# Kernel optimization log

Measured on AMD Instinct MI355X. Metric: run time of the kernel, lower is better.

## Reference

```python
import jax, jax.numpy as jnp
import numpy as np

DECAY = 0.9
THRESH = 1.0
ALPHA = 4.0  # surrogate-gradient sharpness for the LIF heaviside
NUM_HEADS = 8


def lif(x):
    """LIF neuron over leading time axis: mem = decay*mem + x; spike = H(mem - thresh); soft reset.
    Forward emits the hard spike; a sigmoid surrogate carries the gradient (straight-through).
    x: (T, M, D) -> spikes (T, M, D)."""
    def step(mem, xt):
        mem = DECAY * mem + xt
        sg = jax.nn.sigmoid(ALPHA * (mem - THRESH))
        hard = (mem >= THRESH).astype(xt.dtype)
        spike = sg + jax.lax.stop_gradient(hard - sg)
        mem = mem - spike * THRESH
        return mem, spike
    _, spikes = jax.lax.scan(step, jnp.zeros_like(x[0]), x)
    return spikes


def setup_inputs() -> dict:
    key = jax.random.key(0)
    ks = jax.random.split(key, 6)
    T, B, N, D = 4, 16, 1024, 512
    s = 1.0 / np.sqrt(D)
    return {
        "x_seq": jax.random.normal(ks[0], (T, B, N, D), jnp.float32),
        "Wq": (jax.random.normal(ks[1], (D, D), jnp.float32) * s),
        "Wk": (jax.random.normal(ks[2], (D, D), jnp.float32) * s),
        "Wv": (jax.random.normal(ks[3], (D, D), jnp.float32) * s),
        "Wp": (jax.random.normal(ks[4], (D, D), jnp.float32) * s),
        "bp": jnp.zeros((D,), jnp.float32),
    }


def reference(x_seq, Wq, Wk, Wv, Wp, bp):
    T, B, N, D = x_seq.shape
    hd = D // NUM_HEADS
    xf = x_seq.reshape(T, B * N, D)
    # projections (no bias) + LIF spiking, then the module's view into (T,B,H,N,hd)
    q = lif(xf @ Wq.T).reshape(T, B, NUM_HEADS, N, hd)
    k = lif(xf @ Wk.T).reshape(T, B, NUM_HEADS, N, hd)
    v = lif(xf @ Wv.T).reshape(T, B, NUM_HEADS, N, hd)
    # causal linear attention: elementwise kv, cumulative sum over time (kv_state is None on fresh module)
    context = jnp.cumsum(k * v, axis=0)
    out = (q * context).reshape(T, B * N, D)
    return (out @ Wp.T + bp).reshape(T, B, N, D)
```

## Files before the change

kernel.cpp:

```cpp
#include <hip/hip_runtime.h>
#include <hip/hip_bf16.h>
#include <stdint.h>

#define T_ 4
#define M_ 16384
#define D_ 512
#define R_ (T_ * M_)
#define EPS_TRIG 1e-4f

typedef short bf16x8 __attribute__((ext_vector_type(8)));
typedef float f32x4  __attribute__((ext_vector_type(4)));
typedef unsigned short us8 __attribute__((ext_vector_type(8)));

static __device__ __forceinline__ void split2bf16(float x, unsigned short& h, unsigned short& l) {
    unsigned int u = __float_as_uint(x);
    h = (unsigned short)(u >> 16);
    float r = x - __uint_as_float(u & 0xFFFF0000u);
    unsigned int v = __float_as_uint(r);
    l = (unsigned short)((v + 0x7FFFu + ((v >> 16) & 1u)) >> 16);
}

static __device__ __forceinline__ void gload_lds16(const void* g, void* l) {
    __builtin_amdgcn_global_load_lds(
        (const __attribute__((address_space(1))) unsigned int*)g,
        (__attribute__((address_space(3))) unsigned int*)l,
        16, 0, 0);
}

__global__ __launch_bounds__(256) void split_w_tiled(
    const float* __restrict__ Wq, const float* __restrict__ Wk, const float* __restrict__ Wv,
    unsigned short* __restrict__ Wt)
{
    const int flat = blockIdx.x * 256 + threadIdx.x;
    const int dd   = flat & 63;
    const int rest = flat >> 6;
    const int wj   = rest % 24;
    const int bk   = rest / 24;
    const int kbi  = bk & 15;
    const int bd   = bk >> 4;
    const int z    = wj % 3;
    const int hg   = wj / 3;
    const int hl   = hg >> 2;
    const int g    = hg & 3;

    const float* src = ((z == 0) ? Wq : (z == 1) ? Wk : Wv)
                       + (size_t)(bd * 64 + dd) * D_ + kbi * 32 + g * 8;
    float4 a = *reinterpret_cast<const float4*>(src);
    float4 b = *reinterpret_cast<const float4*>(src + 4);

    us8 hv, lv;
    unsigned short hh, ll;
    split2bf16(a.x, hh, ll); hv[0] = hh; lv[0] = ll;
    split2bf16(a.y, hh, ll); hv[1] = hh; lv[1] = ll;
    split2bf16(a.z, hh, ll); hv[2] = hh; lv[2] = ll;
    split2bf16(a.w, hh, ll); hv[3] = hh; lv[3] = ll;
    split2bf16(b.x, hh, ll); hv[4] = hh; lv[4] = ll;
    split2bf16(b.y, hh, ll); hv[5] = hh; lv[5] = ll;
    split2bf16(b.z, hh, ll); hv[6] = hh; lv[6] = ll;
    split2bf16(b.w, hh, ll); hv[7] = hh; lv[7] = ll;

    *reinterpret_cast<us8*>((char*)Wt + (size_t)flat * 16) = hl ? lv : hv;
}

__global__ __launch_bounds__(256) void split_wp_tiled(
    const float* __restrict__ Wp, unsigned short* __restrict__ WpT)
{
    const int flat = blockIdx.x * 256 + threadIdx.x;
    const int dd   = flat & 63;
    const int g    = (flat >> 6) & 3;
    const int kbi  = (flat >> 8) & 15;
    const int bd   = flat >> 12;

    const float* src = Wp + (size_t)(bd * 64 + dd) * D_ + kbi * 32 + g * 8;
    float4 a = *reinterpret_cast<const float4*>(src);
    float4 b = *reinterpret_cast<const float4*>(src + 4);

    us8 hv, lv;
    unsigned short hh, ll;
    split2bf16(a.x, hh, ll); hv[0] = hh; lv[0] = ll;
    split2bf16(a.y, hh, ll); hv[1] = hh; lv[1] = ll;
    split2bf16(a.z, hh, ll); hv[2] = hh; lv[2] = ll;
    split2bf16(a.w, hh, ll); hv[3] = hh; lv[3] = ll;
    split2bf16(b.x, hh, ll); hv[4] = hh; lv[4] = ll;
    split2bf16(b.y, hh, ll); hv[5] = hh; lv[5] = ll;
    split2bf16(b.z, hh, ll); hv[6] = hh; lv[6] = ll;
    split2bf16(b.w, hh, ll); hv[7] = hh; lv[7] = ll;

    char* chunk = (char*)WpT + (size_t)(bd * 16 + kbi) * 8192;
    *reinterpret_cast<us8*>(chunk + g * 1024 + dd * 16)        = hv;
    *reinterpret_cast<us8*>(chunk + 4096 + g * 1024 + dd * 16) = lv;
}

__global__ __launch_bounds__(256) void split_x_tiled3(
    const float* __restrict__ X, unsigned short* __restrict__ Xt)
{
    const int bmp  = blockIdx.x;
    const int tid  = threadIdx.x;
    const int rowp = tid >> 2;
    const int g    = tid & 3;
    const int t    = rowp >> 4;
    const int mm   = rowp & 15;

    const float* srow = X + (size_t)(t * M_ + bmp * 16 + mm) * D_;

    for (int kb = 0; kb < 16; kb++) {
        const float* src = srow + kb * 32 + g * 8;
        float4 a = *reinterpret_cast<const float4*>(src);
        float4 b = *reinterpret_cast<const float4*>(src + 4);

        us8 hv, lv;
        unsigned short hh, ll;
        split2bf16(a.x, hh, ll); hv[0] = hh; lv[0] = ll;
        split2bf16(a.y, hh, ll); hv[1] = hh; lv[1] = ll;
        split2bf16(a.z, hh, ll); hv[2] = hh; lv[2] = ll;
        split2bf16(a.w, hh, ll); hv[3] = hh; lv[3] = ll;
        split2bf16(b.x, hh, ll); hv[4] = hh; lv[4] = ll;
        split2bf16(b.y, hh, ll); hv[5] = hh; lv[5] = ll;
        split2bf16(b.z, hh, ll); hv[6] = hh; lv[6] = ll;
        split2bf16(b.w, hh, ll); hv[7] = hh; lv[7] = ll;

        char* chunk = (char*)Xt + (size_t)(bmp * 16 + kb) * 8192;
        *reinterpret_cast<us8*>(chunk + g * 1024 + rowp * 16)        = hv;
        *reinterpret_cast<us8*>(chunk + 4096 + g * 1024 + rowp * 16) = lv;
    }
}

__global__ __launch_bounds__(256, 4) void proj_lif_attn_v5(
    const float* __restrict__ X,
    const float* __restrict__ Wq, const float* __restrict__ Wk, const float* __restrict__ Wv,
    const unsigned short* __restrict__ XtS, const unsigned short* __restrict__ WtS,
    unsigned char* __restrict__ attn)
{
    __shared__ unsigned short Xs[2][4096];

    const int tid  = threadIdx.x;
    const int lane = tid & 63;
    const int wsub = tid >> 6;
    const int la   = lane & 15;
    const int lq   = lane >> 4;

    const int n   = blockIdx.y * 8 + blockIdx.x;
    const int bd  = (n >> 3) & 7;
    const int bmp = (n & 7) * 128 + (n >> 6);

    f32x4 acc[3][T_];
    #pragma unroll
    for (int z = 0; z < 3; z++)
        #pragma unroll
        for (int t = 0; t < T_; t++)
            acc[z][t] = (f32x4){0.f, 0.f, 0.f, 0.f};

    const char* xsrc0 = (const char*)XtS + (size_t)(bmp * 16) * 8192 + wsub * 2048 + lane * 16;
    const char* wb    = (const char*)WtS + (size_t)(bd * 16) * 24576 + lq * 3072 + wsub * 256 + la * 16;
    char* xd0 = (char*)&Xs[0][0] + wsub * 2048;
    char* xd1 = (char*)&Xs[1][0] + wsub * 2048;

    bf16x8 whA[3], wlA[3], whB[3], wlB[3];

    auto loadW = [&](bf16x8 (&wh)[3], bf16x8 (&wl)[3], int kbi) {
        const char* p = wb + (size_t)kbi * 24576;
        #pragma unroll
        for (int z = 0; z < 3; z++) {
            wh[z] = *reinterpret_cast<const bf16x8*>(p + z * 1024);
            wl[z] = *reinterpret_cast<const bf16x8*>(p + z * 1024 + 12288);
        }
    };
    auto stageX = [&](int kbi, char* xd) {
        const char* xs = xsrc0 + (size_t)kbi * 8192;
        gload_lds16(xs,        xd);
        gload_lds16(xs + 1024, xd + 1024);
    };
    auto mfmaPhase = [&](const unsigned short* Xc, const bf16x8 (&wh)[3], const bf16x8 (&wl)[3]) {
        #pragma unroll
        for (int t = 0; t < T_; t++) {
            const int ab = lq * 1024 + (t * 16 + la) * 16;
            bf16x8 ah = *reinterpret_cast<const bf16x8*>((const char*)Xc + ab);
            bf16x8 al = *reinterpret_cast<const bf16x8*>((const char*)Xc + 4096 + ab);
            #pragma unroll
            for (int z = 0; z < 3; z++) {
                acc[z][t] = __builtin_amdgcn_mfma_f32_16x16x32_bf16(ah, wh[z], acc[z][t], 0, 0, 0);
                acc[z][t] = __builtin_amdgcn_mfma_f32_16x16x32_bf16(ah, wl[z], acc[z][t], 0, 0, 0);
                acc[z][t] = __builtin_amdgcn_mfma_f32_16x16x32_bf16(al, wh[z], acc[z][t], 0, 0, 0);
            }
        }
    };

    stageX(0, xd0);
    loadW(whA, wlA, 0);
    __syncthreads();

    for (int kp = 0; kp < 8; kp++) {
        stageX(2 * kp + 1, xd1);
        loadW(whB, wlB, 2 * kp + 1);
        mfmaPhase(&Xs[0][0], whA, wlA);
        __syncthreads();
        if (kp < 7) {
            stageX(2 * kp + 2, xd0);
            loadW(whA, wlA, 2 * kp + 2);
        }
        mfmaPhase(&Xs[1][0], whB, wlB);
        __syncthreads();
    }

    const int d = bd * 64 + wsub * 16 + la;
    #pragma unroll
    for (int i = 0; i < 4; i++) {
        const int m = bmp * 16 + lq * 4 + i;
        int sp[3][T_];
        int zrisky = 0;
        #pragma unroll
        for (int z = 0; z < 3; z++) {
            float mem = 0.f;
            #pragma unroll
            for (int t = 0; t < T_; t++) {
                mem = 0.9f * mem + acc[z][t][i];
                if (fabsf(mem - 1.0f) < EPS_TRIG) zrisky |= (1 << z);
                const int sb = (mem >= 1.0f) ? 1 : 0;
                sp[z][t] = sb;
                mem -= (float)sb;
            }
        }
        unsigned long long ball = __ballot(zrisky != 0);
        while (ball) {
            const int src = (int)__builtin_ctzll(ball);
            ball &= ball - 1;
            const int bits = __shfl(zrisky, src);
            const int m_s  = bmp * 16 + (src >> 4) * 4 + i;
            const int d_s  = bd * 64 + wsub * 16 + (src & 15);
            #pragma unroll
            for (int z = 0; z < 3; z++) {
                if (!(bits & (1 << z))) continue;
                const float* Wrow = ((z == 0) ? Wq : (z == 1) ? Wk : Wv) + (size_t)d_s * D_;
                float4 w0 = *reinterpret_cast<const float4*>(Wrow + lane * 8);
                float4 w1 = *reinterpret_cast<const float4*>(Wrow + lane * 8 + 4);
                double pre[T_];
                #pragma unroll
                for (int t = 0; t < T_; t++) {
                    const float* xrow = X + (size_t)(t * M_ + m_s) * D_ + lane * 8;
                    float4 x0 = *reinterpret_cast<const float4*>(xrow);
                    float4 x1 = *reinterpret_cast<const float4*>(xrow + 4);
                    double p = (double)x0.x * (double)w0.x + (double)x0.y * (double)w0.y
                             + (double)x0.z * (double)w0.z + (double)x0.w * (double)w0.w
                             + (double)x1.x * (double)w1.x + (double)x1.y * (double)w1.y
                             + (double)x1.z * (double)w1.z + (double)x1.w * (double)w1.w;
                    #pragma unroll
                    for (int off = 32; off > 0; off >>= 1)
                        p += __shfl_xor(p, off, 64);
                    pre[t] = p;
                }
                double dm = 0.0;
                int spz[T_];
                #pragma unroll
                for (int t = 0; t < T_; t++) {
                    dm = 0.9 * dm + pre[t];
                    const int sb = (dm >= 1.0) ? 1 : 0;
                    spz[t] = sb;
                    dm -= (double)sb;
                }
                if (lane == src) {
                    #pragma unroll
                    for (int t = 0; t < T_; t++) sp[z][t] = spz[t];
                }
            }
        }
        int ctx = 0;
        #pragma unroll
        for (int t = 0; t < T_; t++) {
            ctx += sp[1][t] & sp[2][t];
            attn[(size_t)(t * M_ + m) * D_ + d] = (unsigned char)(sp[0][t] ? ctx : 0);
        }
    }
}

__global__ __launch_bounds__(256, 4) void attn_out_gemm_v3(
    const unsigned char* __restrict__ A,
    const unsigned short* __restrict__ WpT,
    const float*         __restrict__ bp,
    float* __restrict__ out)
{
    __shared__ unsigned short As[2][128 * 40];

    const int tid  = threadIdx.x;
    const int lane = tid & 63;
    const int wsub = tid >> 6;
    const int la   = lane & 15;
    const int lq   = lane >> 4;

    const int n  = blockIdx.y * 8 + blockIdx.x;
    const int bd = (n >> 3) & 7;
    const int bm = (n & 7) * 64 + (n >> 6);

    f32x4 acc[8];
    #pragma unroll
    for (int s = 0; s < 8; s++) acc[s] = (f32x4){0.f, 0.f, 0.f, 0.f};

    int arow[4], akq[4];
    #pragma unroll
    for (int i = 0; i < 4; i++) {
        const int j = tid + i * 256;
        arow[i] = j >> 3;
        akq[i]  = (j & 7) * 4;
    }
    const unsigned char* Ab = A + (size_t)(bm * 128) * D_;

    uchar4 S[4], P[4];
    bf16x8 whA, wlA, whB, wlB;

    auto loadA = [&](uchar4 (&r)[4], int kb) {
        #pragma unroll
        for (int i = 0; i < 4; i++)
            r[i] = *reinterpret_cast<const uchar4*>(
                Ab + (size_t)arow[i] * D_ + kb * 32 + akq[i]);
    };
    auto storeA = [&](int buf, const uchar4 (&r)[4]) {
        #pragma unroll
        for (int i = 0; i < 4; i++) {
            ushort4 h;
            h.x = (unsigned short)(__float_as_uint((float)r[i].x) >> 16);
            h.y = (unsigned short)(__float_as_uint((float)r[i].y) >> 16);
            h.z = (unsigned short)(__float_as_uint((float)r[i].z) >> 16);
            h.w = (unsigned short)(__float_as_uint((float)r[i].w) >> 16);
            *reinterpret_cast<ushort4*>(&As[buf][arow[i] * 40 + akq[i]]) = h;
        }
    };
    auto loadW = [&](bf16x8& wh, bf16x8& wl, int kb) {
        const char* p = (const char*)WpT + (size_t)(bd * 16 + kb) * 8192
                        + lq * 1024 + (wsub * 16 + la) * 16;
        wh = *reinterpret_cast<const bf16x8*>(p);
        wl = *reinterpret_cast<const bf16x8*>(p + 4096);
    };
    auto mfmaPhase = [&](int buf, const bf16x8& wh, const bf16x8& wl) {
        #pragma unroll
        for (int s = 0; s < 8; s++) {
            bf16x8 a = *reinterpret_cast<const bf16x8*>(&As[buf][(s * 16 + la) * 40 + lq * 8]);
            acc[s] = __builtin_amdgcn_mfma_f32_16x16x32_bf16(a, wh, acc[s], 0, 0, 0);
            acc[s] = __builtin_amdgcn_mfma_f32_16x16x32_bf16(a, wl, acc[s], 0, 0, 0);
        }
    };

    loadA(S, 0);
    storeA(0, S);
    loadW(whA, wlA, 0);
    loadA(S, 1);
    __syncthreads();

    for (int kp = 0; kp < 8; kp++) {
        storeA(1, S);
        loadW(whB, wlB, 2 * kp + 1);
        if (kp < 7) loadA(P, 2 * kp + 2);
        mfmaPhase(0, whA, wlA);
        __syncthreads();
        if (kp < 7) {
            storeA(0, P);
            loadW(whA, wlA, 2 * kp + 2);
            loadA(S, 2 * kp + 3);
        }
        mfmaPhase(1, whB, wlB);
        __syncthreads();
    }

    const int d = bd * 64 + wsub * 16 + la;
    const float bias = bp[d];
    #pragma unroll
    for (int s = 0; s < 8; s++)
        #pragma unroll
        for (int i = 0; i < 4; i++) {
            const int m = bm * 128 + s * 16 + lq * 4 + i;
            out[(size_t)m * D_ + d] = acc[s][i] + bias;
        }
}

extern "C" void kernel_launch(void* const* d_in, const int* in_sizes, int n_in,
                              void* d_out, int out_size, void* d_ws, size_t ws_size,
                              hipStream_t stream) {
    const float* x  = (const float*)d_in[0];
    const float* wq = (const float*)d_in[1];
    const float* wk = (const float*)d_in[2];
    const float* wv = (const float*)d_in[3];
    const float* wp = (const float*)d_in[4];
    const float* bp = (const float*)d_in[5];

    unsigned char*  attn = (unsigned char*)d_ws;
    unsigned short* Wt   = (unsigned short*)((char*)d_ws + 33554432);
    unsigned short* WpT  = (unsigned short*)((char*)d_ws + 36700160);
    unsigned short* Xt   = (unsigned short*)((char*)d_ws + 37748736);

    dim3 blk(256);
    split_w_tiled <<<dim3(768),  blk, 0, stream>>>(wq, wk, wv, Wt);
    split_wp_tiled<<<dim3(128),  blk, 0, stream>>>(wp, WpT);
    split_x_tiled3<<<dim3(1024), blk, 0, stream>>>(x, Xt);

    dim3 g1(8, 1024);
    proj_lif_attn_v5<<<g1, blk, 0, stream>>>(x, wq, wk, wv, Xt, Wt, attn);

    dim3 g2(8, 512);
    attn_out_gemm_v3<<<g2, blk, 0, stream>>>(attn, WpT, bp, (float*)d_out);
}
```

Measured before the change: 549.3 us.

## Fuse X bf16 split into projection kernel and emit pre-tiled bf16 attention

```diff
diff --git a/kernel.cpp b/kernel.cpp
--- a/kernel.cpp
+++ b/kernel.cpp
@@ -18,6 +18,18 @@
     float r = x - __uint_as_float(u & 0xFFFF0000u);
     unsigned int v = __float_as_uint(r);
     l = (unsigned short)((v + 0x7FFFu + ((v >> 16) & 1u)) >> 16);
+}
+
+static __device__ __forceinline__ void split8(const float4& a, const float4& b, us8& hv, us8& lv) {
+    unsigned short hh, ll;
+    split2bf16(a.x, hh, ll); hv[0] = hh; lv[0] = ll;
+    split2bf16(a.y, hh, ll); hv[1] = hh; lv[1] = ll;
+    split2bf16(a.z, hh, ll); hv[2] = hh; lv[2] = ll;
+    split2bf16(a.w, hh, ll); hv[3] = hh; lv[3] = ll;
+    split2bf16(b.x, hh, ll); hv[4] = hh; lv[4] = ll;
+    split2bf16(b.y, hh, ll); hv[5] = hh; lv[5] = ll;
+    split2bf16(b.z, hh, ll); hv[6] = hh; lv[6] = ll;
+    split2bf16(b.w, hh, ll); hv[7] = hh; lv[7] = ll;
 }
 
 static __device__ __forceinline__ void gload_lds16(const void* g, void* l) {
@@ -47,18 +59,8 @@
                        + (size_t)(bd * 64 + dd) * D_ + kbi * 32 + g * 8;
     float4 a = *reinterpret_cast<const float4*>(src);
     float4 b = *reinterpret_cast<const float4*>(src + 4);
-
     us8 hv, lv;
-    unsigned short hh, ll;
-    split2bf16(a.x, hh, ll); hv[0] = hh; lv[0] = ll;
-    split2bf16(a.y, hh, ll); hv[1] = hh; lv[1] = ll;
-    split2bf16(a.z, hh, ll); hv[2] = hh; lv[2] = ll;
-    split2bf16(a.w, hh, ll); hv[3] = hh; lv[3] = ll;
-    split2bf16(b.x, hh, ll); hv[4] = hh; lv[4] = ll;
-    split2bf16(b.y, hh, ll); hv[5] = hh; lv[5] = ll;
-    split2bf16(b.z, hh, ll); hv[6] = hh; lv[6] = ll;
-    split2bf16(b.w, hh, ll); hv[7] = hh; lv[7] = ll;
-
+    split8(a, b, hv, lv);
     *reinterpret_cast<us8*>((char*)Wt + (size_t)flat * 16) = hl ? lv : hv;
 }
 
@@ -74,62 +76,18 @@
     const float* src = Wp + (size_t)(bd * 64 + dd) * D_ + kbi * 32 + g * 8;
     float4 a = *reinterpret_cast<const float4*>(src);
     float4 b = *reinterpret_cast<const float4*>(src + 4);
-
     us8 hv, lv;
-    unsigned short hh, ll;
-    split2bf16(a.x, hh, ll); hv[0] = hh; lv[0] = ll;
-    split2bf16(a.y, hh, ll); hv[1] = hh; lv[1] = ll;
-    split2bf16(a.z, hh, ll); hv[2] = hh; lv[2] = ll;
-    split2bf16(a.w, hh, ll); hv[3] = hh; lv[3] = ll;
-    split2bf16(b.x, hh, ll); hv[4] = hh; lv[4] = ll;
-    split2bf16(b.y, hh, ll); hv[5] = hh; lv[5] = ll;
-    split2bf16(b.z, hh, ll); hv[6] = hh; lv[6] = ll;
-    split2bf16(b.w, hh, ll); hv[7] = hh; lv[7] = ll;
-
+    split8(a, b, hv, lv);
     char* chunk = (char*)WpT + (size_t)(bd * 16 + kbi) * 8192;
     *reinterpret_cast<us8*>(chunk + g * 1024 + dd * 16)        = hv;
     *reinterpret_cast<us8*>(chunk + 4096 + g * 1024 + dd * 16) = lv;
 }
 
-__global__ __launch_bounds__(256) void split_x_tiled3(
-    const float* __restrict__ X, unsigned short* __restrict__ Xt)
-{
-    const int bmp  = blockIdx.x;
-    const int tid  = threadIdx.x;
-    const int rowp = tid >> 2;
-    const int g    = tid & 3;
-    const int t    = rowp >> 4;
-    const int mm   = rowp & 15;
-
-    const float* srow = X + (size_t)(t * M_ + bmp * 16 + mm) * D_;
-
-    for (int kb = 0; kb < 16; kb++) {
-        const float* src = srow + kb * 32 + g * 8;
-        float4 a = *reinterpret_cast<const float4*>(src);
-        float4 b = *reinterpret_cast<const float4*>(src + 4);
-
-        us8 hv, lv;
-        unsigned short hh, ll;
-        split2bf16(a.x, hh, ll); hv[0] = hh; lv[0] = ll;
-        split2bf16(a.y, hh, ll); hv[1] = hh; lv[1] = ll;
-        split2bf16(a.z, hh, ll); hv[2] = hh; lv[2] = ll;
-        split2bf16(a.w, hh, ll); hv[3] = hh; lv[3] = ll;
-        split2bf16(b.x, hh, ll); hv[4] = hh; lv[4] = ll;
-        split2bf16(b.y, hh, ll); hv[5] = hh; lv[5] = ll;
-        split2bf16(b.z, hh, ll); hv[6] = hh; lv[6] = ll;
-        split2bf16(b.w, hh, ll); hv[7] = hh; lv[7] = ll;
-
-        char* chunk = (char*)Xt + (size_t)(bmp * 16 + kb) * 8192;
-        *reinterpret_cast<us8*>(chunk + g * 1024 + rowp * 16)        = hv;
-        *reinterpret_cast<us8*>(chunk + 4096 + g * 1024 + rowp * 16) = lv;
-    }
-}
-
-__global__ __launch_bounds__(256, 4) void proj_lif_attn_v5(
+__global__ __launch_bounds__(256, 4) void proj_lif_attn_v6(
     const float* __restrict__ X,
     const float* __restrict__ Wq, const float* __restrict__ Wk, const float* __restrict__ Wv,
-    const unsigned short* __restrict__ XtS, const unsigned short* __restrict__ WtS,
-    unsigned char* __restrict__ attn)
+    const unsigned short* __restrict__ WtS,
+    unsigned short* __restrict__ attnT)
 {
     __shared__ unsigned short Xs[2][4096];
 
@@ -150,12 +108,18 @@
         for (int t = 0; t < T_; t++)
             acc[z][t] = (f32x4){0.f, 0.f, 0.f, 0.f};
 
-    const char* xsrc0 = (const char*)XtS + (size_t)(bmp * 16) * 8192 + wsub * 2048 + lane * 16;
-    const char* wb    = (const char*)WtS + (size_t)(bd * 16) * 24576 + lq * 3072 + wsub * 256 + la * 16;
-    char* xd0 = (char*)&Xs[0][0] + wsub * 2048;
-    char* xd1 = (char*)&Xs[1][0] + wsub * 2048;
+    const int srow = tid & 63;
+    const int sg   = tid >> 6;
+    const int st   = srow >> 4;
+    const int smm  = srow & 15;
+    const float* xsrc = X + (size_t)(st * M_ + bmp * 16 + smm) * D_ + sg * 8;
+    char* xw0 = (char*)&Xs[0][0] + sg * 1024 + srow * 16;
+    char* xw1 = (char*)&Xs[1][0] + sg * 1024 + srow * 16;
+
+    const char* wb = (const char*)WtS + (size_t)(bd * 16) * 24576 + lq * 3072 + wsub * 256 + la * 16;
 
     bf16x8 whA[3], wlA[3], whB[3], wlB[3];
+    float4 S0, S1, P0, P1;
 
     auto loadW = [&](bf16x8 (&wh)[3], bf16x8 (&wl)[3], int kbi) {
         const char* p = wb + (size_t)kbi * 24576;
@@ -165,10 +129,15 @@
             wl[z] = *reinterpret_cast<const bf16x8*>(p + z * 1024 + 12288);
         }
     };
-    auto stageX = [&](int kbi, char* xd) {
-        const char* xs = xsrc0 + (size_t)kbi * 8192;
-        gload_lds16(xs,        xd);
-        gload_lds16(xs + 1024, xd + 1024);
+    auto loadX = [&](float4& a, float4& b, int kbi) {
+        a = *reinterpret_cast<const float4*>(xsrc + kbi * 32);
+        b = *reinterpret_cast<const float4*>(xsrc + kbi * 32 + 4);
+    };
+    auto storeX = [&](char* dst, const float4& a, const float4& b) {
+        us8 hv, lv;
+        split8(a, b, hv, lv);
+        *reinterpret_cast<us8*>(dst)        = hv;
+        *reinterpret_cast<us8*>(dst + 4096) = lv;
     };
     auto mfmaPhase = [&](const unsigned short* Xc, const bf16x8 (&wh)[3], const bf16x8 (&wl)[3]) {
         #pragma unroll
@@ -185,18 +154,22 @@
         }
     };
 
-    stageX(0, xd0);
+    loadX(S0, S1, 0);
+    storeX(xw0, S0, S1);
     loadW(whA, wlA, 0);
+    loadX(S0, S1, 1);
     __syncthreads();
 
     for (int kp = 0; kp < 8; kp++) {
-        stageX(2 * kp + 1, xd1);
+        storeX(xw1, S0, S1);
         loadW(whB, wlB, 2 * kp + 1);
+        if (kp < 7) loadX(P0, P1, 2 * kp + 2);
         mfmaPhase(&Xs[0][0], whA, wlA);
         __syncthreads();
         if (kp < 7) {
-            stageX(2 * kp + 2, xd0);
+            storeX(xw0, P0, P1);
             loadW(whA, wlA, 2 * kp + 2);
+            loadX(S0, S1, 2 * kp + 3);
         }
         mfmaPhase(&Xs[1][0], whB, wlB);
         __syncthreads();
@@ -263,22 +236,27 @@
                 }
             }
         }
+        const size_t dpart = (size_t)(d >> 5) * 8192 + ((d >> 3) & 3) * 2048 + (d & 7) * 2;
         int ctx = 0;
         #pragma unroll
         for (int t = 0; t < T_; t++) {
             ctx += sp[1][t] & sp[2][t];
-            attn[(size_t)(t * M_ + m) * D_ + d] = (unsigned char)(sp[0][t] ? ctx : 0);
+            const int r = t * M_ + m;
+            const int v = sp[0][t] ? ctx : 0;
+            const unsigned short bv = (unsigned short)(__float_as_uint((float)v) >> 16);
+            *(unsigned short*)((char*)attnT + (size_t)(r >> 7) * 131072
+                               + (size_t)(r & 127) * 16 + dpart) = bv;
         }
     }
 }
 
-__global__ __launch_bounds__(256, 4) void attn_out_gemm_v3(
-    const unsigned char* __restrict__ A,
+__global__ __launch_bounds__(256, 4) void attn_out_gemm_v4(
+    const unsigned short* __restrict__ AT,
     const unsigned short* __restrict__ WpT,
     const float*         __restrict__ bp,
     float* __restrict__ out)
 {
-    __shared__ unsigned short As[2][128 * 40];
+    __shared__ unsigned short As[2][4096];
 
     const int tid  = threadIdx.x;
     const int lane = tid & 63;
@@ -294,34 +272,16 @@
     #pragma unroll
     for (int s = 0; s < 8; s++) acc[s] = (f32x4){0.f, 0.f, 0.f, 0.f};
 
-    int arow[4], akq[4];
-    #pragma unroll
-    for (int i = 0; i < 4; i++) {
-        const int j = tid + i * 256;
-        arow[i] = j >> 3;
-        akq[i]  = (j & 7) * 4;
-    }
-    const unsigned char* Ab = A + (size_t)(bm * 128) * D_;
-
-    uchar4 S[4], P[4];
+    const char* asrc0 = (const char*)AT + (size_t)(bm * 16) * 8192 + wsub * 2048 + lane * 16;
+    char* ad0 = (char*)&As[0][0] + wsub * 2048;
+    char* ad1 = (char*)&As[1][0] + wsub * 2048;
+
     bf16x8 whA, wlA, whB, wlB;
 
-    auto loadA = [&](uchar4 (&r)[4], int kb) {
-        #pragma unroll
-        for (int i = 0; i < 4; i++)
-            r[i] = *reinterpret_cast<const uchar4*>(
-                Ab + (size_t)arow[i] * D_ + kb * 32 + akq[i]);
-    };
-    auto storeA = [&](int buf, const uchar4 (&r)[4]) {
-        #pragma unroll
-        for (int i = 0; i < 4; i++) {
-            ushort4 h;
-            h.x = (unsigned short)(__float_as_uint((float)r[i].x) >> 16);
-            h.y = (unsigned short)(__float_as_uint((float)r[i].y) >> 16);
-            h.z = (unsigned short)(__float_as_uint((float)r[i].z) >> 16);
-            h.w = (unsigned short)(__float_as_uint((float)r[i].w) >> 16);
-            *reinterpret_cast<ushort4*>(&As[buf][arow[i] * 40 + akq[i]]) = h;
-        }
+    auto stageA = [&](int kb, char* xd) {
+        const char* s = asrc0 + (size_t)kb * 8192;
+        gload_lds16(s,        xd);
+        gload_lds16(s + 1024, xd + 1024);
     };
     auto loadW = [&](bf16x8& wh, bf16x8& wl, int kb) {
         const char* p = (const char*)WpT + (size_t)(bd * 16 + kb) * 8192
@@ -329,33 +289,30 @@
         wh = *reinterpret_cast<const bf16x8*>(p);
         wl = *reinterpret_cast<const bf16x8*>(p + 4096);
     };
-    auto mfmaPhase = [&](int buf, const bf16x8& wh, const bf16x8& wl) {
+    auto mfmaPhase = [&](const unsigned short* Ac, const bf16x8& wh, const bf16x8& wl) {
         #pragma unroll
         for (int s = 0; s < 8; s++) {
-            bf16x8 a = *reinterpret_cast<const bf16x8*>(&As[buf][(s * 16 + la) * 40 + lq * 8]);
+            bf16x8 a = *reinterpret_cast<const bf16x8*>(
+                (const char*)Ac + lq * 2048 + (s * 16 + la) * 16);
             acc[s] = __builtin_amdgcn_mfma_f32_16x16x32_bf16(a, wh, acc[s], 0, 0, 0);
             acc[s] = __builtin_amdgcn_mfma_f32_16x16x32_bf16(a, wl, acc[s], 0, 0, 0);
         }
     };
 
-    loadA(S, 0);
-    storeA(0, S);
+    stageA(0, ad0);
     loadW(whA, wlA, 0);
-    loadA(S, 1);
     __syncthreads();
 
     for (int kp = 0; kp < 8; kp++) {
-        storeA(1, S);
+        stageA(2 * kp + 1, ad1);
         loadW(whB, wlB, 2 * kp + 1);
-        if (kp < 7) loadA(P, 2 * kp + 2);
-        mfmaPhase(0, whA, wlA);
+        mfmaPhase(&As[0][0], whA, wlA);
         __syncthreads();
         if (kp < 7) {
-            storeA(0, P);
+            stageA(2 * kp + 2, ad0);
             loadW(whA, wlA, 2 * kp + 2);
-            loadA(S, 2 * kp + 3);
-        }
-        mfmaPhase(1, whB, wlB);
+        }
+        mfmaPhase(&As[1][0], whB, wlB);
         __syncthreads();
     }
 
@@ -365,8 +322,8 @@
     for (int s = 0; s < 8; s++)
         #pragma unroll
         for (int i = 0; i < 4; i++) {
-            const int m = bm * 128 + s * 16 + lq * 4 + i;
-            out[(size_t)m * D_ + d] = acc[s][i] + bias;
+            const int r = bm * 128 + s * 16 + lq * 4 + i;
+            out[(size_t)r * D_ + d] = acc[s][i] + bias;
         }
 }
 
@@ -380,19 +337,17 @@
     const float* wp = (const float*)d_in[4];
     const float* bp = (const float*)d_in[5];
 
-    unsigned char*  attn = (unsigned char*)d_ws;
-    unsigned short* Wt   = (unsigned short*)((char*)d_ws + 33554432);
-    unsigned short* WpT  = (unsigned short*)((char*)d_ws + 36700160);
-    unsigned short* Xt   = (unsigned short*)((char*)d_ws + 37748736);
+    unsigned short* attnT = (unsigned short*)d_ws;
+    unsigned short* Wt    = (unsigned short*)((char*)d_ws + 67108864);
+    unsigned short* WpT   = (unsigned short*)((char*)d_ws + 67108864 + 3145728);
 
     dim3 blk(256);
-    split_w_tiled <<<dim3(768),  blk, 0, stream>>>(wq, wk, wv, Wt);
-    split_wp_tiled<<<dim3(128),  blk, 0, stream>>>(wp, WpT);
-    split_x_tiled3<<<dim3(1024), blk, 0, stream>>>(x, Xt);
+    split_w_tiled <<<dim3(768), blk, 0, stream>>>(wq, wk, wv, Wt);
+    split_wp_tiled<<<dim3(128), blk, 0, stream>>>(wp, WpT);
 
     dim3 g1(8, 1024);
-    proj_lif_attn_v5<<<g1, blk, 0, stream>>>(x, wq, wk, wv, Xt, Wt, attn);
+    proj_lif_attn_v6<<<g1, blk, 0, stream>>>(x, wq, wk, wv, Wt, attnT);
 
     dim3 g2(8, 512);
-    attn_out_gemm_v3<<<g2, blk, 0, stream>>>(attn, WpT, bp, (float*)d_out);
-}
+    attn_out_gemm_v4<<<g2, blk, 0, stream>>>(attnT, WpT, bp, (float*)d_out);
+}
```

After: 648.8 us. 1.18x slower.
